# Kernel tuning notes

Measured on AMD Instinct MI355X. Metric: run time of the kernel, lower is better.

The kernel has to match this reference:

```python
import jax, jax.numpy as jnp
import numpy as np
import math

D_MODEL = 1024
FEAT = 16            # feature_dim
HEADS = 16
HEAD_DIM = D_MODEL // HEADS          # 64
EXP = 1 + FEAT + FEAT * FEAT         # 273, expanded (Taylor) feature dim
BATCH = 4
SEQ = 2048


def taylor_exp(x):
    """2nd-order Taylor feature map: [1, x/d^{1/4}, (x ox x)/(sqrt(2)*sqrt(d))]."""
    d = x.shape[-1]
    r2 = math.sqrt(2.0)
    rd = math.sqrt(d)
    rrd = math.sqrt(rd)
    x2 = (x[..., :, None] * x[..., None, :]).reshape(*x.shape[:-1], d * d) / r2
    return jnp.concatenate([jnp.ones_like(x[..., :1]), x / rrd, x2 / rd], axis=-1)


def setup_inputs() -> dict:
    key = jax.random.key(0)
    ks = jax.random.split(key, 9)
    s_in = 1.0 / math.sqrt(D_MODEL)
    inp = {
        "x": jax.random.normal(ks[0], (BATCH, SEQ, D_MODEL), dtype=jnp.float32),
        "kv_state": jnp.zeros((BATCH, HEADS, EXP, HEAD_DIM), dtype=jnp.float32),
        "k_state": jnp.zeros((BATCH, HEADS, EXP), dtype=jnp.float32),
        # Linear params stored as [in, out] (y = x @ W + b)
        "Wq": jax.random.normal(ks[1], (D_MODEL, FEAT * HEADS), dtype=jnp.float32) * s_in,
        "bq": jnp.zeros((FEAT * HEADS,), dtype=jnp.float32),
        "Wk": jax.random.normal(ks[2], (D_MODEL, FEAT * HEADS), dtype=jnp.float32) * s_in,
        "bk": jnp.zeros((FEAT * HEADS,), dtype=jnp.float32),
        "Wv": jax.random.normal(ks[3], (D_MODEL, HEAD_DIM * HEADS), dtype=jnp.float32) * s_in,
        "bv": jnp.zeros((HEAD_DIM * HEADS,), dtype=jnp.float32),
        "Wo": jax.random.normal(ks[4], (HEADS * HEAD_DIM, D_MODEL), dtype=jnp.float32) * s_in,
        "bo": jnp.zeros((D_MODEL,), dtype=jnp.float32),
    }
    return inp


def _forward(x, kv_state, k_state, Wq, bq, Wk, bk, Wv, bv, Wo, bo):
    b, l, _ = x.shape
    # projections -> b h l d
    q = (x @ Wq + bq).reshape(b, l, HEADS, FEAT).transpose(0, 2, 1, 3)
    k = (x @ Wk + bk).reshape(b, l, HEADS, FEAT).transpose(0, 2, 1, 3)
    v = (x @ Wv + bv).reshape(b, l, HEADS, HEAD_DIM).transpose(0, 2, 1, 3)
    q = taylor_exp(q)  # b h l EXP
    k = taylor_exp(k)  # b h l EXP

    # scan over time: carry (kv_state [b,h,EXP,hd], k_state [b,h,EXP])
    qs = jnp.moveaxis(q, 2, 0)  # l b h EXP
    ks = jnp.moveaxis(k, 2, 0)  # l b h EXP
    vs = jnp.moveaxis(v, 2, 0)  # l b h hd

    def step(carry, qkv_t):
        kv, kst = carry
        q_t, k_t, v_t = qkv_t
        kv = kv + k_t[..., :, None] * v_t[..., None, :]   # b h EXP hd
        kst = kst + k_t                                    # b h EXP
        num = jnp.einsum('bhd,bhdc->bhc', q_t, kv)
        den = jnp.einsum('bhd,bhd->bh', q_t, kst) + 1e-6
        return (kv, kst), num / den[..., None]

    (kv_f, kst_f), outs = jax.lax.scan(step, (kv_state, k_state), (qs, ks, vs))
    # outs: l b h hd -> b l (h hd)
    y = jnp.moveaxis(outs, 0, 1).reshape(b, l, HEADS * HEAD_DIM)
    y = y @ Wo + bo  # dropout is identity in eval mode
    return y, kv_f, kst_f


def reference(x, kv_state, k_state, Wq, bq, Wk, bk, Wv, bv, Wo, bo):
    return _forward(x, kv_state, k_state, Wq, bq, Wk, bk, Wv, bv, Wo, bo)
```

## Files before the change

### kernel.cpp

```cpp
#include <hip/hip_runtime.h>

typedef unsigned short u16;
typedef __attribute__((ext_vector_type(8))) short bf16x8;
typedef __attribute__((ext_vector_type(4))) float f32x4;

#define BATCH 4
#define SEQ   2048
#define DM    1024
#define HEADS 16
#define FEAT  16
#define HD    64
#define EXPD  273
#define EXPP  288
#define CHK   128
#define NC    16
#define BH    64
#define QKS   512
#define MROWS 8192
#define C2    0.17677669529663687f

__device__ __forceinline__ u16 f2b(float f) {
  union { float f; unsigned u; } v; v.f = f;
  unsigned u = v.u;
  return (u16)((u + 0x7fffu + ((u >> 16) & 1u)) >> 16);
}
__device__ __forceinline__ float b2f(u16 s) {
  union { unsigned u; float f; } v; v.u = ((unsigned)s) << 16; return v.f;
}

typedef const unsigned int __attribute__((address_space(1)))* gas1;
typedef unsigned int __attribute__((address_space(3)))* las3;
__device__ __forceinline__ void gl_lds16(const u16* g, u16* l) {
  __builtin_amdgcn_global_load_lds((gas1)(const void*)g, (las3)(void*)l, 16, 0, 0);
}

__global__ __launch_bounds__(256) void prep(const float* __restrict__ x, u16* __restrict__ xb,
                                            const float* __restrict__ Wq, const float* __restrict__ Wk,
                                            const float* __restrict__ Wv, const float* __restrict__ Wo,
                                            u16* __restrict__ wqkT, u16* __restrict__ wvT, u16* __restrict__ woT,
                                            const float* __restrict__ bq, const float* __restrict__ bk,
                                            float* __restrict__ bqk) {
  __shared__ float tile[32][33];
  int id = blockIdx.x;
  if (id < 8192) {
    int i = id * 256 + threadIdx.x;
    float4 v = ((const float4*)x)[i];
    u16 r[4] = {f2b(v.x), f2b(v.y), f2b(v.z), f2b(v.w)};
    ((uint2*)xb)[i] = *(uint2*)r;
    return;
  }
  id -= 8192;
  if (id < 2560) {
    const float* src; u16* dst; int N, t;
    if (id < 256)       { src = Wq; dst = wqkT;            N = 256;  t = id; }
    else if (id < 512)  { src = Wk; dst = wqkT + 256 * DM; N = 256;  t = id - 256; }
    else if (id < 1536) { src = Wv; dst = wvT;             N = 1024; t = id - 512; }
    else                { src = Wo; dst = woT;             N = 1024; t = id - 1536; }
    int nt = N / 32;
    int n0 = (t % nt) * 32, k0 = (t / nt) * 32;
    int tx = threadIdx.x & 31, ty = threadIdx.x >> 5;
    for (int i = ty; i < 32; i += 8)
      tile[i][tx] = src[(size_t)(k0 + i) * N + n0 + tx];
    __syncthreads();
    for (int i = ty; i < 32; i += 8)
      dst[(size_t)(n0 + i) * DM + k0 + tx] = f2b(tile[tx][i]);
    return;
  }
  int i = threadIdx.x;
  bqk[i] = bq[i];
  bqk[256 + i] = bk[i];
}

__global__ __launch_bounds__(256) void gemm128(const u16* __restrict__ A, const u16* __restrict__ BT,
                                               const float* __restrict__ bias, int M, int N, int K,
                                               float* __restrict__ outF, u16* __restrict__ outB,
                                               u16* __restrict__ outT) {
  __shared__ __align__(16) u16 As[128 * 32];
  __shared__ __align__(16) u16 Bs[128 * 32];
  const int tid = threadIdx.x;
  const int wave = tid >> 6, lane = tid & 63, qd = lane >> 4, ln = lane & 15;
  const int wr = (wave >> 1) * 64, wc = (wave & 1) * 64;
  const int m0 = blockIdx.y * 128, n0 = blockIdx.x * 128;
  f32x4 acc[4][4];
#pragma unroll
  for (int i = 0; i < 4; i++)
#pragma unroll
    for (int j = 0; j < 4; j++) acc[i][j] = (f32x4){0.f, 0.f, 0.f, 0.f};
  const int sr = tid >> 2, sk = (tid & 3) * 8;
  const u16* gA0 = A + (size_t)(m0 + sr) * K + sk;
  const u16* gA1 = A + (size_t)(m0 + 64 + sr) * K + sk;
  const u16* gB0 = BT + (size_t)(n0 + sr) * K + sk;
  const u16* gB1 = BT + (size_t)(n0 + 64 + sr) * K + sk;
  u16* lA0 = &As[(size_t)(wave * 64) * 8];
  u16* lA1 = &As[(size_t)(256 + wave * 64) * 8];
  u16* lB0 = &Bs[(size_t)(wave * 64) * 8];
  u16* lB1 = &Bs[(size_t)(256 + wave * 64) * 8];
  for (int kk = 0; kk < K; kk += 32) {
    gl_lds16(gA0 + kk, lA0);
    gl_lds16(gA1 + kk, lA1);
    gl_lds16(gB0 + kk, lB0);
    gl_lds16(gB1 + kk, lB1);
    __syncthreads();
    bf16x8 af[4], bf[4];
#pragma unroll
    for (int t = 0; t < 4; t++) {
      af[t] = *(const bf16x8*)&As[(wr + t * 16 + ln) * 32 + qd * 8];
      bf[t] = *(const bf16x8*)&Bs[(wc + t * 16 + ln) * 32 + qd * 8];
    }
#pragma unroll
    for (int mt = 0; mt < 4; mt++)
#pragma unroll
      for (int nt = 0; nt < 4; nt++)
        acc[mt][nt] = __builtin_amdgcn_mfma_f32_16x16x32_bf16(af[mt], bf[nt], acc[mt][nt], 0, 0, 0);
    __syncthreads();
  }
  if (outT) {
#pragma unroll
    for (int nt = 0; nt < 4; nt++) {
      int col = n0 + wc + nt * 16 + ln;
      float bv = bias[col];
#pragma unroll
      for (int mt = 0; mt < 4; mt++) {
        u16 pk[4];
#pragma unroll
        for (int r = 0; r < 4; r++) pk[r] = f2b(acc[mt][nt][r] + bv);
        int row0 = m0 + wr + mt * 16 + qd * 4;
        *(uint2*)&outT[(size_t)col * M + row0] = *(uint2*)pk;
      }
    }
    return;
  }
#pragma unroll
  for (int nt = 0; nt < 4; nt++) {
    int col = n0 + wc + nt * 16 + ln;
    float bv = bias[col];
#pragma unroll
    for (int mt = 0; mt < 4; mt++) {
#pragma unroll
      for (int r = 0; r < 4; r++) {
        int row = m0 + wr + mt * 16 + qd * 4 + r;
        float v = acc[mt][nt][r] + bv;
        if (outF) outF[(size_t)row * N + col] = v;
        else      outB[(size_t)row * N + col] = f2b(v);
      }
    }
  }
}

__global__ __launch_bounds__(256) void chunk_sums(const float* __restrict__ qkw, const u16* __restrict__ vbT,
                                                  u16* __restrict__ ckvT, float* __restrict__ ck) {
  __shared__ float kl[CHK][17];
  __shared__ __align__(16) u16 kfT[4][16][136];
  const int tid = threadIdx.x;
  const int bh = blockIdx.x / NC, c = blockIdx.x % NC;
  const int b = bh >> 4, h = bh & 15;
  const int wave = tid >> 6, lane = tid & 63, qd = lane >> 4, ln = lane & 15;
  const size_t rowbase = (size_t)(b * SEQ + c * CHK);
#pragma unroll
  for (int it = 0; it < 2; it++) {
    int i = tid + it * 256;
    int tt = i >> 2, f0 = (i & 3) * 4;
    float4 v = *(const float4*)&qkw[(rowbase + tt) * QKS + 256 + h * FEAT + f0];
    kl[tt][f0] = v.x; kl[tt][f0 + 1] = v.y; kl[tt][f0 + 2] = v.z; kl[tt][f0 + 3] = v.w;
  }
  uint4 bVv[4][4];
#pragma unroll
  for (int kk2 = 0; kk2 < 4; kk2++)
#pragma unroll
    for (int nt = 0; nt < 4; nt++)
      bVv[kk2][nt] = *(const uint4*)&vbT[(size_t)(h * HD + nt * 16 + ln) * MROWS +
                                         rowbase + kk2 * 32 + qd * 8];
  __syncthreads();
  const size_t obase = (size_t)(bh * NC + c) * HD;
  for (int mt = wave; mt < 18; mt += 4) {
#pragma unroll
    for (int el = 0; el < 16; el++) {
      int e = mt * 16 + el;
#pragma unroll
      for (int hh = 0; hh < 2; hh++) {
        int t = lane + hh * 64;
        float val;
        if (e == 0) val = 1.0f;
        else if (e < 17) val = 0.5f * kl[t][e - 1];
        else if (e < EXPD) { int u = e - 17; val = C2 * kl[t][u >> 4] * kl[t][u & 15]; }
        else val = 0.0f;
        kfT[wave][el][t] = f2b(val);
      }
    }
    f32x4 acc[4];
#pragma unroll
    for (int nt = 0; nt < 4; nt++) acc[nt] = (f32x4){0.f, 0.f, 0.f, 0.f};
#pragma unroll
    for (int kk2 = 0; kk2 < 4; kk2++) {
      bf16x8 a = *(const bf16x8*)&kfT[wave][ln][kk2 * 32 + qd * 8];
#pragma unroll
      for (int nt = 0; nt < 4; nt++) {
        bf16x8 bb = *(const bf16x8*)&bVv[kk2][nt];
        acc[nt] = __builtin_amdgcn_mfma_f32_16x16x32_bf16(a, bb, acc[nt], 0, 0, 0);
      }
    }
#pragma unroll
    for (int nt = 0; nt < 4; nt++) {
      u16 pk[4];
#pragma unroll
      for (int r = 0; r < 4; r++) pk[r] = f2b(acc[nt][r]);
      *(uint2*)&ckvT[(obase + nt * 16 + ln) * EXPP + mt * 16 + qd * 4] = *(uint2*)pk;
    }
  }
  for (int e = tid; e < EXPP; e += 256) {
    float s = 0.f;
    if (e == 0) s = (float)CHK;
    else if (e < 17) { float t = 0.f; for (int tt = 0; tt < CHK; tt++) t += kl[tt][e - 1]; s = 0.5f * t; }
    else if (e < EXPD) {
      int u = e - 17, i0 = u >> 4, j0 = u & 15; float t = 0.f;
      for (int tt = 0; tt < CHK; tt++) t += kl[tt][i0] * kl[tt][j0];
      s = C2 * t;
    }
    ck[(size_t)(bh * NC + c) * EXPP + e] = s;
  }
}

__global__ __launch_bounds__(256) void kv_prefix(u16* __restrict__ ckvT, const float* __restrict__ kv0,
                                                 float* __restrict__ out_kv,
                                                 float* __restrict__ ck, const float* __restrict__ k0,
                                                 float* __restrict__ out_k) {
  const int tid = threadIdx.x;
  const int bh = blockIdx.x / 10, eg = blockIdx.x % 10;
  if (eg == 9) {
    for (int e = tid; e < EXPP; e += 256) {
      float S = (e < EXPD) ? k0[(size_t)bh * EXPD + e] : 0.f;
      for (int c = 0; c < NC; c++) {
        size_t idx = ((size_t)bh * NC + c) * EXPP + e;
        float v = ck[idx];
        ck[idx] = S;
        S += v;
      }
      if (e < EXPD) out_k[(size_t)bh * EXPD + e] = S;
    }
    return;
  }
  const int hd = tid >> 2;
  const int e0 = eg * 32 + (tid & 3) * 8;
  float S[8];
#pragma unroll
  for (int j = 0; j < 8; j++) {
    int e = e0 + j;
    S[j] = (e < EXPD) ? kv0[((size_t)bh * EXPD + e) * HD + hd] : 0.f;
  }
  u16* base = ckvT + ((size_t)bh * NC * HD + hd) * EXPP + e0;
  const size_t cstride = (size_t)HD * EXPP;
  uint4 v0 = *(const uint4*)base;
  uint4 v1 = *(const uint4*)(base + cstride);
  for (int c = 0; c < NC; c++) {
    uint4 vn = v1;
    if (c + 2 < NC) vn = *(const uint4*)(base + (size_t)(c + 2) * cstride);
    union { uint4 q; u16 s[8]; } pk;
#pragma unroll
    for (int j = 0; j < 8; j++) pk.s[j] = f2b(S[j]);
    *(uint4*)(base + (size_t)c * cstride) = pk.q;
    union { uint4 q; u16 s[8]; } vv; vv.q = v0;
#pragma unroll
    for (int j = 0; j < 8; j++) S[j] += b2f(vv.s[j]);
    v0 = v1; v1 = vn;
  }
#pragma unroll
  for (int j = 0; j < 8; j++) {
    int e = e0 + j;
    if (e < EXPD) out_kv[((size_t)bh * EXPD + e) * HD + hd] = S[j];
  }
}

__global__ __launch_bounds__(256) void out_chunk(const float* __restrict__ qkw, const u16* __restrict__ vbT,
                                                 const u16* __restrict__ ckvT, const float* __restrict__ ck,
                                                 u16* __restrict__ ob) {
  __shared__ float ql[CHK][17];
  __shared__ __align__(16) u16 pool[4 * CHK * 40];
  __shared__ float kstl[EXPP];
  __shared__ float denl[CHK];
  u16 (*qlb)[40] = (u16(*)[40])pool;
  u16 (*klb)[40] = (u16(*)[40])(pool + CHK * 40);
  u16 (*qfs)[CHK][40] = (u16(*)[CHK][40])(pool + 2 * CHK * 40);
  u16 (*al)[136] = (u16(*)[136])pool;
  const int tid = threadIdx.x;
  const int bh = blockIdx.x / NC, c = blockIdx.x % NC;
  const int b = bh >> 4, h = bh & 15;
  const int wave = tid >> 6, lane = tid & 63, qd = lane >> 4, ln = lane & 15;
  const size_t rowbase = (size_t)(b * SEQ + c * CHK);
#pragma unroll
  for (int it = 0; it < 2; it++) {
    int i = tid + it * 256;
    int tt = i >> 2, f0 = (i & 3) * 4;
    float4 vq = *(const float4*)&qkw[(rowbase + tt) * QKS + h * FEAT + f0];
    float4 vk = *(const float4*)&qkw[(rowbase + tt) * QKS + 256 + h * FEAT + f0];
    ql[tt][f0] = vq.x; ql[tt][f0 + 1] = vq.y; ql[tt][f0 + 2] = vq.z; ql[tt][f0 + 3] = vq.w;
    u16 qb[4] = {f2b(vq.x), f2b(vq.y), f2b(vq.z), f2b(vq.w)};
    u16 kb[4] = {f2b(vk.x), f2b(vk.y), f2b(vk.z), f2b(vk.w)};
    *(uint2*)&qlb[tt][f0] = *(uint2*)qb;
    *(uint2*)&klb[tt][f0] = *(uint2*)kb;
    *(uint2*)&qlb[tt][16 + f0] = (uint2){0u, 0u};
    *(uint2*)&klb[tt][16 + f0] = (uint2){0u, 0u};
  }
  const size_t cbase = (size_t)(bh * NC + c);
  for (int e = tid; e < EXPP; e += 256) kstl[e] = ck[cbase * EXPP + e];
  const u16* sptr = ckvT + (cbase * HD + wave * 16 + ln) * EXPP + qd * 8;
  uint4 bSv[9];
#pragma unroll
  for (int kt = 0; kt < 9; kt++) bSv[kt] = *(const uint4*)(sptr + kt * 32);
  uint4 bVv[4];
#pragma unroll
  for (int kk2 = 0; kk2 < 4; kk2++)
    bVv[kk2] = *(const uint4*)&vbT[(size_t)(h * HD + wave * 16 + ln) * MROWS +
                                   rowbase + kk2 * 32 + qd * 8];
  auto feat = [&](int buf, int kt) {
#pragma unroll
    for (int ii = 0; ii < 16; ii++) {
      int i = tid + ii * 256;
      int tt = i >> 5, el = i & 31;
      int e = kt * 32 + el;
      float qv;
      if (e == 0) qv = 1.f;
      else if (e < 17) qv = 0.5f * ql[tt][e - 1];
      else if (e < EXPD) { int u = e - 17; qv = C2 * ql[tt][u >> 4] * ql[tt][u & 15]; }
      else qv = 0.f;
      qfs[buf][tt][el] = f2b(qv);
    }
  };
  __syncthreads();
  feat(0, 0);
  __syncthreads();
  f32x4 accO[8];
#pragma unroll
  for (int mt = 0; mt < 8; mt++) accO[mt] = (f32x4){0.f, 0.f, 0.f, 0.f};
  for (int kt = 0; kt < 9; kt++) {
    int cur = kt & 1;
    if (kt < 8) feat(cur ^ 1, kt + 1);
    bf16x8 bS = *(const bf16x8*)&bSv[kt];
#pragma unroll
    for (int mt = 0; mt < 8; mt++) {
      bf16x8 a = *(const bf16x8*)&qfs[cur][mt * 16 + ln][qd * 8];
      accO[mt] = __builtin_amdgcn_mfma_f32_16x16x32_bf16(a, bS, accO[mt], 0, 0, 0);
    }
    __syncthreads();
  }
  f32x4 accU[8][2];
#pragma unroll
  for (int st2 = 0; st2 < 2; st2++) {
    bf16x8 bU = *(const bf16x8*)&klb[(wave + st2 * 4) * 16 + ln][qd * 8];
#pragma unroll
    for (int mt = 0; mt < 8; mt++) {
      bf16x8 aU = *(const bf16x8*)&qlb[mt * 16 + ln][qd * 8];
      accU[mt][st2] = __builtin_amdgcn_mfma_f32_16x16x32_bf16(aU, bU, (f32x4){0.f, 0.f, 0.f, 0.f}, 0, 0, 0);
    }
  }
  __syncthreads();
#pragma unroll
  for (int mt = 0; mt < 8; mt++)
#pragma unroll
    for (int st2 = 0; st2 < 2; st2++)
#pragma unroll
      for (int r = 0; r < 4; r++) {
        int t = mt * 16 + qd * 4 + r, s = (wave + st2 * 4) * 16 + ln;
        float u = accU[mt][st2][r];
        float sc = 1.f + 0.25f * u + 0.03125f * u * u;
        al[t][s] = f2b((s <= t) ? sc : 0.f);
      }
  __syncthreads();
#pragma unroll
  for (int kk2 = 0; kk2 < 4; kk2++) {
    bf16x8 bb = *(const bf16x8*)&bVv[kk2];
#pragma unroll
    for (int mt = 0; mt < 8; mt++) {
      bf16x8 a = *(const bf16x8*)&al[mt * 16 + ln][kk2 * 32 + qd * 8];
      accO[mt] = __builtin_amdgcn_mfma_f32_16x16x32_bf16(a, bb, accO[mt], 0, 0, 0);
    }
  }
  {
    int t = tid >> 1, p = tid & 1;
    float q16[16];
#pragma unroll
    for (int j = 0; j < 16; j++) q16[j] = ql[t][j];
    float s = 0.f;
#pragma unroll
    for (int i2 = 0; i2 < 8; i2++) {
      int i = p * 8 + i2;
      float inner = 0.f;
#pragma unroll
      for (int j = 0; j < 16; j++) inner += q16[j] * kstl[17 + i * 16 + j];
      s += q16[i] * inner;
    }
    s *= C2;
    float s1 = 0.f;
#pragma unroll
    for (int j2 = 0; j2 < 8; j2++) { int j = p * 8 + j2; s1 += q16[j] * kstl[1 + j]; }
    s += 0.5f * s1;
    if (p == 0) s += kstl[0] + 1e-6f;
    float da = 0.f;
    for (int s2 = 0; s2 < 64; s2++) da += b2f(al[t][p * 64 + s2]);
    s += da;
    s += __shfl_xor(s, 1);
    if (p == 0) denl[t] = s;
  }
  __syncthreads();
#pragma unroll
  for (int mt = 0; mt < 8; mt++)
#pragma unroll
    for (int r = 0; r < 4; r++) {
      int t = mt * 16 + qd * 4 + r;
      ob[(rowbase + t) * DM + h * HD + wave * 16 + ln] = f2b(accO[mt][r] / denl[t]);
    }
}

extern "C" void kernel_launch(void* const* d_in, const int* in_sizes, int n_in,
                              void* d_out, int out_size, void* d_ws, size_t ws_size,
                              hipStream_t stream) {
  (void)in_sizes; (void)n_in; (void)out_size;
  const float* x   = (const float*)d_in[0];
  const float* kv0 = (const float*)d_in[1];
  const float* k0  = (const float*)d_in[2];
  const float* bq  = (const float*)d_in[4];
  const float* bk  = (const float*)d_in[6];
  const float* bv  = (const float*)d_in[8];
  const float* bo  = (const float*)d_in[10];
  float* out = (float*)d_out;
  char* ws = (char*)d_ws;
  size_t off = 0;
  auto take = [&](size_t bytes) { char* p = ws + off; off += (bytes + 255) & ~(size_t)255; return p; };
  u16*   xb   = (u16*)  take((size_t)BATCH * SEQ * DM * 2);
  u16*   wqkT = (u16*)  take((size_t)QKS * DM * 2);
  u16*   wvT  = (u16*)  take((size_t)DM * DM * 2);
  u16*   woT  = (u16*)  take((size_t)DM * DM * 2);
  float* bqk  = (float*)take((size_t)QKS * 4);
  float* qkw  = (float*)take((size_t)BATCH * SEQ * QKS * 4);
  u16*   vbT  = (u16*)  take((size_t)BATCH * SEQ * DM * 2);
  u16*   ckvT = (u16*)  take((size_t)BH * NC * EXPP * HD * 2);
  float* ck   = (float*)take((size_t)BH * NC * EXPP * 4);
  u16*   ob   = (u16*)  take((size_t)BATCH * SEQ * DM * 2);
  if (off > ws_size) return;

  float* out_kv = out + (size_t)BATCH * SEQ * DM;
  float* out_k  = out_kv + (size_t)BH * EXPD * HD;

  prep<<<8192 + 2560 + 1, 256, 0, stream>>>(x, xb,
      (const float*)d_in[3], (const float*)d_in[5], (const float*)d_in[7], (const float*)d_in[9],
      wqkT, wvT, woT, bq, bk, bqk);

  gemm128<<<dim3(4, 64), 256, 0, stream>>>(xb, wqkT, bqk, MROWS, QKS, DM, qkw, nullptr, nullptr);
  gemm128<<<dim3(8, 64), 256, 0, stream>>>(xb, wvT,  bv,  MROWS, DM,  DM, nullptr, nullptr, vbT);

  chunk_sums<<<BH * NC, 256, 0, stream>>>(qkw, vbT, ckvT, ck);
  kv_prefix<<<BH * 10, 256, 0, stream>>>(ckvT, kv0, out_kv, ck, k0, out_k);
  out_chunk<<<BH * NC, 256, 0, stream>>>(qkw, vbT, ckvT, ck, ob);

  gemm128<<<dim3(8, 64), 256, 0, stream>>>(ob, woT, bo, MROWS, DM, DM, out, nullptr, nullptr);
}
```

Before: 303.6 us.

## Compute Taylor features per-row in registers with compile-time index maps

Feature-map construction in both chunk_sums and out_chunk is rewritten so each thread pair owns one token row, holds its 16 projected features in registers, and writes 16 contiguous bf16 features via templated, compile-time-indexed code. This replaces per-element branchy index decoding and scattered shared-memory reads. The chunk_sums loop over M tiles is restructured into explicit barrier-separated phases, and the denominator's diagonal-sum reads are vectorized. The intent is to cut ALU and LDS work in the feature expansion, at the cost of extra __syncthreads and more register pressure.

```diff
diff --git a/kernel.cpp b/kernel.cpp
--- a/kernel.cpp
+++ b/kernel.cpp
@@ -147,21 +147,95 @@
   }
 }
 
+template<int KT>
+__device__ __forceinline__ void feat_row(const float* q16, int p, u16* dst) {
+  u16 pk[16];
+  if (KT == 0 && p == 0) {
+    pk[0] = 0x3F80;
+#pragma unroll
+    for (int j = 1; j < 16; j++) pk[j] = f2b(0.5f * q16[j - 1]);
+  } else if (KT == 0) {
+    pk[0] = f2b(0.5f * q16[15]);
+    float wm = C2 * q16[0];
+#pragma unroll
+    for (int j = 1; j < 16; j++) pk[j] = f2b(wm * q16[j - 1]);
+  } else {
+    constexpr int c = 2 * KT;
+    float wm = C2 * (p ? q16[c]     : q16[c - 1]);
+    float w0 = C2 * (p ? q16[c - 1] : q16[c - 2]);
+    pk[0] = f2b(w0 * q16[15]);
+#pragma unroll
+    for (int j = 1; j < 16; j++) pk[j] = f2b(wm * q16[j - 1]);
+    if (KT == 8 && p) {
+#pragma unroll
+      for (int j = 1; j < 16; j++) pk[j] = 0;
+    }
+  }
+  *(uint4*)dst = *(uint4*)pk;
+  *(uint4*)(dst + 8) = *(uint4*)(pk + 8);
+}
+
+template<int MTB>
+__device__ __forceinline__ void kfeat(const float* k16, int p, int t2, u16 (*kfT)[16][136]) {
+  u16 pk[16];
+  if (MTB == 0 && true) {
+    if (p == 0) {
+      pk[0] = 0x3F80;
+#pragma unroll
+      for (int j = 1; j < 16; j++) pk[j] = f2b(0.5f * k16[j - 1]);
+    } else {
+      float w0 = C2 * k16[0], wm = C2 * k16[1];
+      pk[0] = f2b(w0 * k16[15]);
+#pragma unroll
+      for (int j = 1; j < 16; j++) pk[j] = f2b(wm * k16[j - 1]);
+    }
+  } else if (MTB == 1) {
+    if (p == 0) {
+      pk[0] = f2b(0.5f * k16[15]);
+      float wm = C2 * k16[0];
+#pragma unroll
+      for (int j = 1; j < 16; j++) pk[j] = f2b(wm * k16[j - 1]);
+    } else {
+      float w0 = C2 * k16[1], wm = C2 * k16[2];
+      pk[0] = f2b(w0 * k16[15]);
+#pragma unroll
+      for (int j = 1; j < 16; j++) pk[j] = f2b(wm * k16[j - 1]);
+    }
+  } else {
+    float wm = C2 * (p ? k16[MTB + 1] : k16[MTB - 1]);
+    float w0 = C2 * (p ? k16[MTB]     : k16[MTB - 2]);
+    pk[0] = f2b(w0 * k16[15]);
+#pragma unroll
+    for (int j = 1; j < 16; j++) pk[j] = f2b(wm * k16[j - 1]);
+  }
+  int b = 2 * p + (MTB & 1);
+#pragma unroll
+  for (int el = 0; el < 16; el++) kfT[b][el][t2] = pk[el];
+}
+
 __global__ __launch_bounds__(256) void chunk_sums(const float* __restrict__ qkw, const u16* __restrict__ vbT,
                                                   u16* __restrict__ ckvT, float* __restrict__ ck) {
-  __shared__ float kl[CHK][17];
+  __shared__ float kl[CHK][20];
   __shared__ __align__(16) u16 kfT[4][16][136];
   const int tid = threadIdx.x;
   const int bh = blockIdx.x / NC, c = blockIdx.x % NC;
   const int b = bh >> 4, h = bh & 15;
   const int wave = tid >> 6, lane = tid & 63, qd = lane >> 4, ln = lane & 15;
+  const int t2 = tid >> 1, p = tid & 1;
   const size_t rowbase = (size_t)(b * SEQ + c * CHK);
-#pragma unroll
-  for (int it = 0; it < 2; it++) {
-    int i = tid + it * 256;
-    int tt = i >> 2, f0 = (i & 3) * 4;
-    float4 v = *(const float4*)&qkw[(rowbase + tt) * QKS + 256 + h * FEAT + f0];
-    kl[tt][f0] = v.x; kl[tt][f0 + 1] = v.y; kl[tt][f0 + 2] = v.z; kl[tt][f0 + 3] = v.w;
+  float k16[16];
+  {
+    const float* kp = &qkw[(rowbase + t2) * QKS + 256 + h * FEAT];
+    float4 v0 = *(const float4*)kp, v1 = *(const float4*)(kp + 4);
+    float4 v2 = *(const float4*)(kp + 8), v3 = *(const float4*)(kp + 12);
+    k16[0] = v0.x; k16[1] = v0.y; k16[2] = v0.z; k16[3] = v0.w;
+    k16[4] = v1.x; k16[5] = v1.y; k16[6] = v1.z; k16[7] = v1.w;
+    k16[8] = v2.x; k16[9] = v2.y; k16[10] = v2.z; k16[11] = v2.w;
+    k16[12] = v3.x; k16[13] = v3.y; k16[14] = v3.z; k16[15] = v3.w;
+    float4 h0, h1;
+    if (p == 0) { h0 = v0; h1 = v1; } else { h0 = v2; h1 = v3; }
+    *(float4*)&kl[t2][p * 8] = h0;
+    *(float4*)&kl[t2][p * 8 + 4] = h1;
   }
   uint4 bVv[4][4];
 #pragma unroll
@@ -170,29 +244,14 @@
     for (int nt = 0; nt < 4; nt++)
       bVv[kk2][nt] = *(const uint4*)&vbT[(size_t)(h * HD + nt * 16 + ln) * MROWS +
                                          rowbase + kk2 * 32 + qd * 8];
-  __syncthreads();
   const size_t obase = (size_t)(bh * NC + c) * HD;
-  for (int mt = wave; mt < 18; mt += 4) {
-#pragma unroll
-    for (int el = 0; el < 16; el++) {
-      int e = mt * 16 + el;
-#pragma unroll
-      for (int hh = 0; hh < 2; hh++) {
-        int t = lane + hh * 64;
-        float val;
-        if (e == 0) val = 1.0f;
-        else if (e < 17) val = 0.5f * kl[t][e - 1];
-        else if (e < EXPD) { int u = e - 17; val = C2 * kl[t][u >> 4] * kl[t][u & 15]; }
-        else val = 0.0f;
-        kfT[wave][el][t] = f2b(val);
-      }
-    }
+  auto mstore = [&](int mt, int bufw) {
     f32x4 acc[4];
 #pragma unroll
     for (int nt = 0; nt < 4; nt++) acc[nt] = (f32x4){0.f, 0.f, 0.f, 0.f};
 #pragma unroll
     for (int kk2 = 0; kk2 < 4; kk2++) {
-      bf16x8 a = *(const bf16x8*)&kfT[wave][ln][kk2 * 32 + qd * 8];
+      bf16x8 a = *(const bf16x8*)&kfT[bufw][ln][kk2 * 32 + qd * 8];
 #pragma unroll
       for (int nt = 0; nt < 4; nt++) {
         bf16x8 bb = *(const bf16x8*)&bVv[kk2][nt];
@@ -206,7 +265,41 @@
       for (int r = 0; r < 4; r++) pk[r] = f2b(acc[nt][r]);
       *(uint2*)&ckvT[(obase + nt * 16 + ln) * EXPP + mt * 16 + qd * 4] = *(uint2*)pk;
     }
-  }
+  };
+  __syncthreads();
+  kfeat<0>(k16, p, t2, kfT); kfeat<1>(k16, p, t2, kfT);
+  __syncthreads();
+  mstore(wave, wave);
+  __syncthreads();
+  kfeat<4>(k16, p, t2, kfT); kfeat<5>(k16, p, t2, kfT);
+  __syncthreads();
+  mstore(4 + wave, wave);
+  __syncthreads();
+  kfeat<8>(k16, p, t2, kfT); kfeat<9>(k16, p, t2, kfT);
+  __syncthreads();
+  mstore(8 + wave, wave);
+  __syncthreads();
+  kfeat<12>(k16, p, t2, kfT); kfeat<13>(k16, p, t2, kfT);
+  __syncthreads();
+  mstore(12 + wave, wave);
+  __syncthreads();
+  {
+    u16 pk[16];
+    if (p == 0) {
+      float w0 = C2 * k16[14], wm = C2 * k16[15];
+      pk[0] = f2b(w0 * k16[15]);
+#pragma unroll
+      for (int j = 1; j < 16; j++) pk[j] = f2b(wm * k16[j - 1]);
+    } else {
+      pk[0] = f2b(C2 * k16[15] * k16[15]);
+#pragma unroll
+      for (int j = 1; j < 16; j++) pk[j] = 0;
+    }
+#pragma unroll
+    for (int el = 0; el < 16; el++) kfT[p][el][t2] = pk[el];
+  }
+  __syncthreads();
+  if (wave < 2) mstore(16 + wave, wave);
   for (int e = tid; e < EXPP; e += 256) {
     float s = 0.f;
     if (e == 0) s = (float)CHK;
@@ -273,7 +366,6 @@
 __global__ __launch_bounds__(256) void out_chunk(const float* __restrict__ qkw, const u16* __restrict__ vbT,
                                                  const u16* __restrict__ ckvT, const float* __restrict__ ck,
                                                  u16* __restrict__ ob) {
-  __shared__ float ql[CHK][17];
   __shared__ __align__(16) u16 pool[4 * CHK * 40];
   __shared__ float kstl[EXPP];
   __shared__ float denl[CHK];
@@ -285,20 +377,28 @@
   const int bh = blockIdx.x / NC, c = blockIdx.x % NC;
   const int b = bh >> 4, h = bh & 15;
   const int wave = tid >> 6, lane = tid & 63, qd = lane >> 4, ln = lane & 15;
+  const int t2 = tid >> 1, p = tid & 1;
   const size_t rowbase = (size_t)(b * SEQ + c * CHK);
-#pragma unroll
-  for (int it = 0; it < 2; it++) {
-    int i = tid + it * 256;
-    int tt = i >> 2, f0 = (i & 3) * 4;
-    float4 vq = *(const float4*)&qkw[(rowbase + tt) * QKS + h * FEAT + f0];
-    float4 vk = *(const float4*)&qkw[(rowbase + tt) * QKS + 256 + h * FEAT + f0];
-    ql[tt][f0] = vq.x; ql[tt][f0 + 1] = vq.y; ql[tt][f0 + 2] = vq.z; ql[tt][f0 + 3] = vq.w;
-    u16 qb[4] = {f2b(vq.x), f2b(vq.y), f2b(vq.z), f2b(vq.w)};
-    u16 kb[4] = {f2b(vk.x), f2b(vk.y), f2b(vk.z), f2b(vk.w)};
-    *(uint2*)&qlb[tt][f0] = *(uint2*)qb;
-    *(uint2*)&klb[tt][f0] = *(uint2*)kb;
-    *(uint2*)&qlb[tt][16 + f0] = (uint2){0u, 0u};
-    *(uint2*)&klb[tt][16 + f0] = (uint2){0u, 0u};
+  float q16[16];
+  {
+    const float* qp = &qkw[(rowbase + t2) * QKS + h * FEAT];
+    float4 v0 = *(const float4*)qp, v1 = *(const float4*)(qp + 4);
+    float4 v2 = *(const float4*)(qp + 8), v3 = *(const float4*)(qp + 12);
+    q16[0] = v0.x; q16[1] = v0.y; q16[2] = v0.z; q16[3] = v0.w;
+    q16[4] = v1.x; q16[5] = v1.y; q16[6] = v1.z; q16[7] = v1.w;
+    q16[8] = v2.x; q16[9] = v2.y; q16[10] = v2.z; q16[11] = v2.w;
+    q16[12] = v3.x; q16[13] = v3.y; q16[14] = v3.z; q16[15] = v3.w;
+    u16 qb[8];
+#pragma unroll
+    for (int j = 0; j < 8; j++) qb[j] = f2b(q16[p * 8 + j]);
+    *(uint4*)&qlb[t2][p * 8] = *(uint4*)qb;
+    *(uint4*)&qlb[t2][16 + p * 8] = (uint4){0u, 0u, 0u, 0u};
+    const float* kp = &qkw[(rowbase + t2) * QKS + 256 + h * FEAT + p * 8];
+    float4 k0v = *(const float4*)kp, k1v = *(const float4*)(kp + 4);
+    u16 kb[8] = {f2b(k0v.x), f2b(k0v.y), f2b(k0v.z), f2b(k0v.w),
+                 f2b(k1v.x), f2b(k1v.y), f2b(k1v.z), f2b(k1v.w)};
+    *(uint4*)&klb[t2][p * 8] = *(uint4*)kb;
+    *(uint4*)&klb[t2][16 + p * 8] = (uint4){0u, 0u, 0u, 0u};
   }
   const size_t cbase = (size_t)(bh * NC + c);
   for (int e = tid; e < EXPP; e += 256) kstl[e] = ck[cbase * EXPP + e];
@@ -311,37 +411,24 @@
   for (int kk2 = 0; kk2 < 4; kk2++)
     bVv[kk2] = *(const uint4*)&vbT[(size_t)(h * HD + wave * 16 + ln) * MROWS +
                                    rowbase + kk2 * 32 + qd * 8];
-  auto feat = [&](int buf, int kt) {
-#pragma unroll
-    for (int ii = 0; ii < 16; ii++) {
-      int i = tid + ii * 256;
-      int tt = i >> 5, el = i & 31;
-      int e = kt * 32 + el;
-      float qv;
-      if (e == 0) qv = 1.f;
-      else if (e < 17) qv = 0.5f * ql[tt][e - 1];
-      else if (e < EXPD) { int u = e - 17; qv = C2 * ql[tt][u >> 4] * ql[tt][u & 15]; }
-      else qv = 0.f;
-      qfs[buf][tt][el] = f2b(qv);
-    }
-  };
-  __syncthreads();
-  feat(0, 0);
+  feat_row<0>(q16, p, &qfs[0][t2][p * 16]);
   __syncthreads();
   f32x4 accO[8];
 #pragma unroll
   for (int mt = 0; mt < 8; mt++) accO[mt] = (f32x4){0.f, 0.f, 0.f, 0.f};
-  for (int kt = 0; kt < 9; kt++) {
-    int cur = kt & 1;
-    if (kt < 8) feat(cur ^ 1, kt + 1);
-    bf16x8 bS = *(const bf16x8*)&bSv[kt];
-#pragma unroll
-    for (int mt = 0; mt < 8; mt++) {
-      bf16x8 a = *(const bf16x8*)&qfs[cur][mt * 16 + ln][qd * 8];
-      accO[mt] = __builtin_amdgcn_mfma_f32_16x16x32_bf16(a, bS, accO[mt], 0, 0, 0);
-    }
-    __syncthreads();
-  }
+#define KSTEP(KT)                                                                          \
+  {                                                                                        \
+    if ((KT) < 8) feat_row<(KT) + 1>(q16, p, &qfs[((KT) + 1) & 1][t2][p * 16]);            \
+    bf16x8 bS = *(const bf16x8*)&bSv[(KT)];                                                \
+    _Pragma("unroll")                                                                      \
+    for (int mt = 0; mt < 8; mt++) {                                                       \
+      bf16x8 a = *(const bf16x8*)&qfs[(KT) & 1][mt * 16 + ln][qd * 8];                     \
+      accO[mt] = __builtin_amdgcn_mfma_f32_16x16x32_bf16(a, bS, accO[mt], 0, 0, 0);        \
+    }                                                                                      \
+    __syncthreads();                                                                       \
+  }
+  KSTEP(0) KSTEP(1) KSTEP(2) KSTEP(3) KSTEP(4) KSTEP(5) KSTEP(6) KSTEP(7) KSTEP(8)
+#undef KSTEP
   f32x4 accU[8][2];
 #pragma unroll
   for (int st2 = 0; st2 < 2; st2++) {
@@ -375,10 +462,6 @@
     }
   }
   {
-    int t = tid >> 1, p = tid & 1;
-    float q16[16];
-#pragma unroll
-    for (int j = 0; j < 16; j++) q16[j] = ql[t][j];
     float s = 0.f;
 #pragma unroll
     for (int i2 = 0; i2 < 8; i2++) {
@@ -391,14 +474,20 @@
     s *= C2;
     float s1 = 0.f;
 #pragma unroll
-    for (int j2 = 0; j2 < 8; j2++) { int j = p * 8 + j2; s1 += q16[j] * kstl[1 + j]; }
+    for (int j2 = 0; j2 < 8; j2++) s1 += q16[p * 8 + j2] * kstl[1 + p * 8 + j2];
     s += 0.5f * s1;
     if (p == 0) s += kstl[0] + 1e-6f;
     float da = 0.f;
-    for (int s2 = 0; s2 < 64; s2++) da += b2f(al[t][p * 64 + s2]);
+#pragma unroll
+    for (int sb = 0; sb < 8; sb++) {
+      union { uint4 q; u16 hh[8]; } uu;
+      uu.q = *(const uint4*)&al[t2][p * 64 + sb * 8];
+#pragma unroll
+      for (int j = 0; j < 8; j++) da += b2f(uu.hh[j]);
+    }
     s += da;
     s += __shfl_xor(s, 1);
-    if (p == 0) denl[t] = s;
+    if (p == 0) denl[t2] = s;
   }
   __syncthreads();
 #pragma unroll
```

After: 305.7 us. Within noise of the previous version (+0.7%).
